# Kernel tuning notes

Measured on AMD Instinct MI355X. Metric: run time of the kernel, lower is better.

The kernel has to match this reference:

```python
import jax, jax.numpy as jnp
import numpy as np

N = 50000        # nodes per type (MiRNA=0, Disease=1, LncRNA=2)
E = 500000       # edges per relation
F_IN, HID, OUT = 128, 64, 64
ITEMS, SIZE, T = 4096, 4096, 100
# relation order: MvsD, DvsM, MvsL, LvsM, LvsD, DvsL
SRC = (0, 1, 0, 2, 2, 1)
DST = (1, 0, 2, 0, 1, 2)


def _sage_hetero_layer(h, edges, Wp, bp, Ws, bs, Wn):
    """One HeteroGraphConv(SAGEConv pool, aggregate='sum') layer.
    h: list of 3 [N, Fin] node-feature arrays; edges: [6, 2, E] int."""
    n = h[0].shape[0]
    out = [None, None, None]
    for e in range(6):
        s, d = SRC[e], DST[e]
        pooled = jax.nn.relu(h[s] @ Wp[e] + bp[e])                 # [N, Fin]
        msg = pooled[edges[e, 0]]                                  # [E, Fin] gather at src
        agg = jax.ops.segment_max(msg, edges[e, 1], num_segments=n)
        agg = jnp.where(jnp.isneginf(agg), 0.0, agg)               # DGL: 0 for isolated dst
        o = h[d] @ Ws[e] + bs[e] + agg @ Wn[e]                     # fc_self(+bias) + fc_neigh
        out[d] = o if out[d] is None else out[d] + o
    return out


def setup_inputs() -> dict:
    key = jax.random.key(0)
    ks = jax.random.split(key, 32)
    s = 0.05
    inp = {
        'hM': jax.random.normal(ks[0], (N, F_IN), jnp.float32),
        'hD': jax.random.normal(ks[1], (N, F_IN), jnp.float32),
        'hL': jax.random.normal(ks[2], (N, F_IN), jnp.float32),
        'Wpool1': jax.random.normal(ks[3], (6, F_IN, F_IN), jnp.float32) * s,
        'bpool1': jnp.zeros((6, F_IN), jnp.float32),
        'Wself1': jax.random.normal(ks[4], (6, F_IN, HID), jnp.float32) * s,
        'bself1': jnp.zeros((6, HID), jnp.float32),
        'Wneigh1': jax.random.normal(ks[5], (6, F_IN, HID), jnp.float32) * s,
        'Wpool2': jax.random.normal(ks[6], (6, HID, HID), jnp.float32) * s,
        'bpool2': jnp.zeros((6, HID), jnp.float32),
        'Wself2': jax.random.normal(ks[7], (6, HID, HID), jnp.float32) * s,
        'bself2': jnp.zeros((6, HID), jnp.float32),
        'Wneigh2': jax.random.normal(ks[8], (6, HID, HID), jnp.float32) * s,
        'Wpool3': jax.random.normal(ks[9], (6, HID, HID), jnp.float32) * s,
        'bpool3': jnp.zeros((6, HID), jnp.float32),
        'Wself3': jax.random.normal(ks[10], (6, HID, OUT), jnp.float32) * s,
        'bself3': jnp.zeros((6, OUT), jnp.float32),
        'Wneigh3': jax.random.normal(ks[11], (6, HID, OUT), jnp.float32) * s,
        'Adj': jax.random.uniform(ks[12], (SIZE, ITEMS), jnp.float32),
        'noise': jax.random.normal(ks[13], (N, OUT), jnp.float32),
        'W1': jax.random.normal(ks[14], (ITEMS + OUT, 256), jnp.float32) * s,
        'b1': jnp.zeros((256,), jnp.float32),
        'W2': jax.random.normal(ks[15], (256, 512), jnp.float32) * s,
        'b2': jnp.zeros((512,), jnp.float32),
        'W3': jax.random.normal(ks[16], (512, 1024), jnp.float32) * s,
        'b3': jnp.zeros((1024,), jnp.float32),
        'W4': jax.random.normal(ks[17], (1024, ITEMS), jnp.float32) * s,
        'b4': jnp.zeros((ITEMS,), jnp.float32),
        'edges': jax.random.randint(ks[18], (6, 2, E), 0, N, jnp.int32),
        't': 50,
        'size': SIZE,
        'leftIndex': 0,
    }
    return inp


def reference(hM, hD, hL, Wpool1, bpool1, Wself1, bself1, Wneigh1,
              Wpool2, bpool2, Wself2, bself2, Wneigh2,
              Wpool3, bpool3, Wself3, bself3, Wneigh3,
              Adj, noise, W1, b1, W2, b2, W3, b3, W4, b4,
              edges, t, size, leftIndex):
    h1 = _sage_hetero_layer([hM, hD, hL], edges, Wpool1, bpool1, Wself1, bself1, Wneigh1)
    h2 = _sage_hetero_layer(h1, edges, Wpool2, bpool2, Wself2, bself2, Wneigh2)
    h3 = _sage_hetero_layer(h2, edges, Wpool3, bpool3, Wself3, bself3, Wneigh3)
    mirna = h3[0]                                                  # [N, OUT]
    mirna = mirna / jnp.maximum(jnp.sum(jnp.abs(mirna), axis=1, keepdims=True), 1e-12)
    # diffusion schedule
    betas = jnp.linspace(1e-4, 0.02, T, dtype=jnp.float32)
    alpha_bars = jnp.cumprod(1.0 - betas)
    signal_rates = jnp.sqrt(alpha_bars)
    noise_rates = jnp.sqrt(1.0 - alpha_bars)
    noisy = signal_rates[t] * mirna + noise_rates[t] * noise
    fake = jax.lax.stop_gradient(noisy[leftIndex:leftIndex + size])  # detach + slice
    M = jnp.concatenate([Adj, fake], axis=1)                       # [size, ITEMS+OUT]
    x = jax.nn.relu(M @ W1 + b1)
    x = jax.nn.relu(x @ W2 + b2)
    x = jax.nn.relu(x @ W3 + b3)
    x = jax.nn.sigmoid(x @ W4 + b4)
    return fake, x
```

## Files before the change

kernel.cpp:

```cpp
#include <hip/hip_runtime.h>
#include <hip/hip_bf16.h>

#define NNODE 50000
#define NEDGE 500000
#define SZ    4096
#define NBKT  256
#define BWID  196
#define BCAP  4096
#define RELEB ((size_t)NBKT * BCAP)
#define ZK1   8

typedef __attribute__((ext_vector_type(8))) short bf16x8;
typedef __attribute__((ext_vector_type(4))) float f32x4;

__device__ __forceinline__ float bits2f(unsigned short u) {
    return __uint_as_float(((unsigned)u) << 16);
}
__device__ __forceinline__ unsigned short f2bits(float f) {
    unsigned x = __float_as_uint(f);
    unsigned r = x + 0x7fffu + ((x >> 16) & 1u);
    return (unsigned short)(r >> 16);
}
__device__ __forceinline__ unsigned pk_max_u16(unsigned a, unsigned b) {
    unsigned lo = max(a & 0xffffu, b & 0xffffu);
    unsigned hi = max(a >> 16, b >> 16);
    return lo | (hi << 16);
}
__device__ __forceinline__ void gl_lds16(const void* g, void* l) {
    __builtin_amdgcn_global_load_lds(
        (const __attribute__((address_space(1))) unsigned int*)g,
        (__attribute__((address_space(3))) unsigned int*)l, 16, 0, 0);
}

template<int RELU, int SIG, int OUTF32, int PART, int PIPE>
__global__ __launch_bounds__(256)
void gemm128(const unsigned short* __restrict__ A, const unsigned short* __restrict__ Bt,
             const float* __restrict__ bias, void* __restrict__ Cv, int M, int N, int K)
{
    __shared__ unsigned short As[PIPE + 1][128 * 64];
    __shared__ unsigned short Bs[PIPE + 1][128 * 64];
    const int tid = threadIdx.x;
    const int wave = tid >> 6, lane = tid & 63;
    const int m16 = lane & 15, quad = lane >> 4;
    const int wr = wave >> 1, wc = wave & 1;
    const int nwg = gridDim.x * gridDim.y;
    int bid = blockIdx.y * gridDim.x + blockIdx.x;
    if ((nwg & 7) == 0) { int cpx = nwg >> 3; bid = (bid & 7) * cpx + (bid >> 3); }
    const int bx = bid % gridDim.x, by = bid / gridDim.x;
    const int row0 = by * 128, col0 = bx * 128;
    const int lrow = lane >> 3, lcol = (lane & 7) * 8;

    f32x4 acc[4][4] = {};

    int k0beg = 0, k0end = K;
    if (PART) {
        const int per = ((K >> 6) + gridDim.z - 1) / gridDim.z;
        k0beg = blockIdx.z * per * 64;
        k0end = min(K, k0beg + per * 64);
    }
    const int nt = (k0end - k0beg) >> 6;

    auto STAGE = [&](int b, int k0) {
#pragma unroll
        for (int i = 0; i < 4; ++i) {
            int chunk = wave * 4 + i;
            int row = chunk * 8 + lrow;
            gl_lds16(A  + (size_t)(row0 + row) * K + k0 + lcol, &As[b][chunk * 512]);
            gl_lds16(Bt + (size_t)(col0 + row) * K + k0 + lcol, &Bs[b][chunk * 512]);
        }
    };
    auto COMPUTE = [&](int b) {
#pragma unroll
        for (int ks = 0; ks < 2; ++ks) {
            bf16x8 a[4], bb[4];
#pragma unroll
            for (int mt = 0; mt < 4; ++mt)
                a[mt] = *(const bf16x8*)&As[b][(wr * 64 + mt * 16 + m16) * 64 + ks * 32 + quad * 8];
#pragma unroll
            for (int nt2 = 0; nt2 < 4; ++nt2)
                bb[nt2] = *(const bf16x8*)&Bs[b][(wc * 64 + nt2 * 16 + m16) * 64 + ks * 32 + quad * 8];
#pragma unroll
            for (int mt = 0; mt < 4; ++mt)
#pragma unroll
                for (int nt2 = 0; nt2 < 4; ++nt2)
                    acc[mt][nt2] = __builtin_amdgcn_mfma_f32_16x16x32_bf16(a[mt], bb[nt2], acc[mt][nt2], 0, 0, 0);
        }
    };

    if (PIPE) {
        STAGE(0, k0beg);
        __syncthreads();
        int cur = 0;
        for (int t = 0; t < nt; ++t) {
            if (t + 1 < nt) STAGE(cur ^ 1, k0beg + (t + 1) * 64);
            COMPUTE(cur);
            __syncthreads();
            cur ^= 1;
        }
    } else {
        for (int t = 0; t < nt; ++t) {
            STAGE(0, k0beg + t * 64);
            __syncthreads();
            COMPUTE(0);
            __syncthreads();
        }
    }

    if (PART) {
        float* P = (float*)Cv + (size_t)blockIdx.z * M * N;
#pragma unroll
        for (int mt = 0; mt < 4; ++mt)
#pragma unroll
            for (int nt2 = 0; nt2 < 4; ++nt2) {
                int gc = col0 + wc * 64 + nt2 * 16 + m16;
#pragma unroll
                for (int r = 0; r < 4; ++r) {
                    int gm = row0 + wr * 64 + mt * 16 + quad * 4 + r;
                    P[(size_t)gm * N + gc] = acc[mt][nt2][r];
                }
            }
        return;
    }

#pragma unroll
    for (int mt = 0; mt < 4; ++mt) {
#pragma unroll
        for (int nt2 = 0; nt2 < 4; ++nt2) {
            int gc = col0 + wc * 64 + nt2 * 16 + m16;
            float bv = bias[gc];
#pragma unroll
            for (int r = 0; r < 4; ++r) {
                int gm = row0 + wr * 64 + mt * 16 + quad * 4 + r;
                size_t idx = (size_t)gm * N + gc;
                float v = acc[mt][nt2][r] + bv;
                if (RELU) v = fmaxf(v, 0.f);
                if (SIG)  v = 1.f / (1.f + __expf(-v));
                if (OUTF32) ((float*)Cv)[idx] = v;
                else        ((unsigned short*)Cv)[idx] = f2bits(v);
            }
        }
    }
}

__global__ __launch_bounds__(256)
void mlp1_ep_k(const float* __restrict__ p, const float* __restrict__ b1,
               unsigned short* __restrict__ x1)
{
    const size_t MN = (size_t)SZ * 256;
    int i = blockIdx.x * 256 + threadIdx.x;
    if (i >= (int)(MN / 4)) return;
    float4 s = ((const float4*)p)[i];
#pragma unroll
    for (int z = 1; z < ZK1; ++z) {
        float4 a = ((const float4*)(p + (size_t)z * MN))[i];
        s.x += a.x; s.y += a.y; s.z += a.z; s.w += a.w;
    }
    int base = i * 4;
    ushort4 o;
    o.x = f2bits(fmaxf(s.x + b1[(base + 0) & 255], 0.f));
    o.y = f2bits(fmaxf(s.y + b1[(base + 1) & 255], 0.f));
    o.z = f2bits(fmaxf(s.z + b1[(base + 2) & 255], 0.f));
    o.w = f2bits(fmaxf(s.w + b1[(base + 3) & 255], 0.f));
    ((ushort4*)x1)[i] = o;
}

template<int NT>
__global__ __launch_bounds__(256)
void pool2_k(const unsigned short* __restrict__ A0, const unsigned short* __restrict__ A1,
             const unsigned short* __restrict__ Bt0, const unsigned short* __restrict__ Bt1,
             const float* __restrict__ b0, const float* __restrict__ b1,
             unsigned short* __restrict__ out, int M, int K)
{
    __shared__ unsigned short As[64][72];
    __shared__ unsigned short Bs[NT * 16][72];
    const int z = blockIdx.z;
    const unsigned short* A = z ? A1 : A0;
    const unsigned short* Bt = z ? Bt1 : Bt0;
    const float* bias = z ? b1 : b0;
    const int N = NT * 16;
    unsigned short* Cv = out + (size_t)z * M * N;

    const int tid = threadIdx.x;
    const int wave = tid >> 6, lane = tid & 63;
    const int m16 = lane & 15, quad = lane >> 4;
    const int row0 = blockIdx.y * 64, col0 = blockIdx.x * N;

    f32x4 acc[NT] = {};

    for (int k0 = 0; k0 < K; k0 += 64) {
#pragma unroll
        for (int it = 0; it < 2; ++it) {
            int u = tid + it * 256;
            int m = u >> 3, c = (u & 7) * 8;
            int gm = row0 + m;
            uint4 v = make_uint4(0u, 0u, 0u, 0u);
            if (gm < M) v = *(const uint4*)(A + (size_t)gm * K + k0 + c);
            *(uint4*)&As[m][c] = v;
        }
#pragma unroll
        for (int it = 0; it < NT / 2; ++it) {
            int u = tid + it * 256;
            int n = u >> 3, c = (u & 7) * 8;
            uint4 v = *(const uint4*)(Bt + (size_t)(col0 + n) * K + k0 + c);
            *(uint4*)&Bs[n][c] = v;
        }
        __syncthreads();
#pragma unroll
        for (int ks = 0; ks < 2; ++ks) {
            bf16x8 a = *(const bf16x8*)&As[wave * 16 + m16][ks * 32 + quad * 8];
#pragma unroll
            for (int nt = 0; nt < NT; ++nt) {
                bf16x8 b = *(const bf16x8*)&Bs[nt * 16 + m16][ks * 32 + quad * 8];
                acc[nt] = __builtin_amdgcn_mfma_f32_16x16x32_bf16(a, b, acc[nt], 0, 0, 0);
            }
        }
        __syncthreads();
    }

#pragma unroll
    for (int nt = 0; nt < NT; ++nt) {
        int gc = col0 + nt * 16 + m16;
        float bv = bias[gc];
#pragma unroll
        for (int r = 0; r < 4; ++r) {
            int gm = row0 + wave * 16 + quad * 4 + r;
            if (gm < M)
                Cv[(size_t)gm * N + gc] = f2bits(fmaxf(acc[nt][r] + bv, 0.f));
        }
    }
}

__global__ __launch_bounds__(256)
void pool6_k(const unsigned short* __restrict__ hin, const unsigned short* __restrict__ pT,
             const float* __restrict__ bp, unsigned short* __restrict__ pooled6, int M)
{
    const int SRCr[6] = {0, 1, 0, 2, 2, 1};
    __shared__ unsigned short As[64][72];
    __shared__ unsigned short Bs[64][72];
    const int z = blockIdx.z;
    const unsigned short* A = hin + (size_t)SRCr[z] * M * 64;
    const unsigned short* Bt = pT + (size_t)z * 4096;
    const float* bias = bp + z * 64;
    unsigned short* Cv = pooled6 + (size_t)z * M * 64;

    const int tid = threadIdx.x;
    const int wave = tid >> 6, lane = tid & 63;
    const int m16 = lane & 15, quad = lane >> 4;
    const int row0 = blockIdx.y * 64;

    f32x4 acc[4] = {};

    {
#pragma unroll
        for (int it = 0; it < 2; ++it) {
            int u = tid + it * 256;
            int m = u >> 3, c = (u & 7) * 8;
            int gm = row0 + m;
            uint4 v = make_uint4(0u, 0u, 0u, 0u);
            if (gm < M) v = *(const uint4*)(A + (size_t)gm * 64 + c);
            *(uint4*)&As[m][c] = v;
        }
#pragma unroll
        for (int it = 0; it < 2; ++it) {
            int u = tid + it * 256;
            int n = u >> 3, c = (u & 7) * 8;
            uint4 v = *(const uint4*)(Bt + (size_t)n * 64 + c);
            *(uint4*)&Bs[n][c] = v;
        }
        __syncthreads();
#pragma unroll
        for (int ks = 0; ks < 2; ++ks) {
            bf16x8 a = *(const bf16x8*)&As[wave * 16 + m16][ks * 32 + quad * 8];
#pragma unroll
            for (int nt = 0; nt < 4; ++nt) {
                bf16x8 b = *(const bf16x8*)&Bs[nt * 16 + m16][ks * 32 + quad * 8];
                acc[nt] = __builtin_amdgcn_mfma_f32_16x16x32_bf16(a, b, acc[nt], 0, 0, 0);
            }
        }
    }

#pragma unroll
    for (int nt = 0; nt < 4; ++nt) {
        int gc = nt * 16 + m16;
        float bv = bias[gc];
#pragma unroll
        for (int r = 0; r < 4; ++r) {
            int gm = row0 + wave * 16 + quad * 4 + r;
            if (gm < M)
                Cv[(size_t)gm * 64 + gc] = f2bits(fmaxf(acc[nt][r] + bv, 0.f));
        }
    }
}

template<int NT>
__global__ __launch_bounds__(256)
void mfma_gemm(const unsigned short* __restrict__ A1, const unsigned short* __restrict__ A2,
               const unsigned short* __restrict__ A3,
               const unsigned short* __restrict__ Bt, const float* __restrict__ bias,
               const float* __restrict__ bias2,
               unsigned short* __restrict__ Cv, int M, int N, int Ka, int Kb, int Kc)
{
    __shared__ unsigned short As[64][72];
    __shared__ unsigned short Bs[NT * 16][72];
    const int tid = threadIdx.x;
    const int wave = tid >> 6, lane = tid & 63;
    const int m16 = lane & 15, quad = lane >> 4;
    const int row0 = blockIdx.y * 64, col0 = blockIdx.x * (NT * 16);
    const int K = Ka + Kb + Kc;

    f32x4 acc[NT] = {};

    for (int k0 = 0; k0 < K; k0 += 64) {
        const int seg = (k0 >= Ka + Kb) ? 2 : ((k0 >= Ka) ? 1 : 0);
        const unsigned short* src = seg == 2 ? A3 : (seg == 1 ? A2 : A1);
        const int ld = seg == 2 ? Kc : (seg == 1 ? Kb : Ka);
        const int kb = k0 - (seg == 2 ? Ka + Kb : (seg == 1 ? Ka : 0));
#pragma unroll
        for (int it = 0; it < 2; ++it) {
            int u = tid + it * 256;
            int m = u >> 3, c = (u & 7) * 8;
            int gm = row0 + m;
            uint4 v = make_uint4(0u, 0u, 0u, 0u);
            if (gm < M) v = *(const uint4*)(src + (size_t)gm * ld + kb + c);
            *(uint4*)&As[m][c] = v;
        }
#pragma unroll
        for (int it = 0; it < NT / 2; ++it) {
            int u = tid + it * 256;
            int n = u >> 3, c = (u & 7) * 8;
            uint4 v = *(const uint4*)(Bt + (size_t)(col0 + n) * K + k0 + c);
            *(uint4*)&Bs[n][c] = v;
        }
        __syncthreads();
#pragma unroll
        for (int ks = 0; ks < 2; ++ks) {
            bf16x8 a = *(const bf16x8*)&As[wave * 16 + m16][ks * 32 + quad * 8];
#pragma unroll
            for (int nt = 0; nt < NT; ++nt) {
                bf16x8 b = *(const bf16x8*)&Bs[nt * 16 + m16][ks * 32 + quad * 8];
                acc[nt] = __builtin_amdgcn_mfma_f32_16x16x32_bf16(a, b, acc[nt], 0, 0, 0);
            }
        }
        __syncthreads();
    }

#pragma unroll
    for (int nt = 0; nt < NT; ++nt) {
        int gc = col0 + nt * 16 + m16;
        float bv = bias[gc] + bias2[gc];
#pragma unroll
        for (int r = 0; r < 4; ++r) {
            int gm = row0 + wave * 16 + quad * 4 + r;
            if (gm < M)
                Cv[(size_t)gm * N + gc] = f2bits(acc[nt][r] + bv);
        }
    }
}

__global__ __launch_bounds__(256)
void fused3_k(const unsigned short* __restrict__ hin,
              const unsigned short* __restrict__ regA, const unsigned short* __restrict__ regB,
              const unsigned short* __restrict__ fT, const float* __restrict__ bs,
              unsigned short* __restrict__ hout, int M)
{
    const int PAe[3] = {1, 0, 2}, PBe[3] = {3, 4, 5};
    __shared__ unsigned short As[64][72];
    __shared__ unsigned short Bs[64][72];
    const int z = blockIdx.z;
    const int eA = PAe[z], eB = PBe[z];
    const unsigned short* A1 = hin + (size_t)z * M * 64;
    const unsigned short* A2 = (eA < 4) ? regA + (size_t)eA * M * 64 : regB + (size_t)(eA - 4) * M * 64;
    const unsigned short* A3 = (eB < 4) ? regA + (size_t)eB * M * 64 : regB + (size_t)(eB - 4) * M * 64;
    const unsigned short* Bt = fT + (size_t)z * 12288;
    const float* bias = bs + eA * 64;
    const float* bias2 = bs + eB * 64;
    unsigned short* Cv = hout + (size_t)z * M * 64;

    const int tid = threadIdx.x;
    const int wave = tid >> 6, lane = tid & 63;
    const int m16 = lane & 15, quad = lane >> 4;
    const int row0 = blockIdx.y * 64;

    f32x4 acc[4] = {};

#pragma unroll
    for (int seg = 0; seg < 3; ++seg) {
        const unsigned short* src = seg == 2 ? A3 : (seg == 1 ? A2 : A1);
        const int k0 = seg * 64;
#pragma unroll
        for (int it = 0; it < 2; ++it) {
            int u = tid + it * 256;
            int m = u >> 3, c = (u & 7) * 8;
            int gm = row0 + m;
            uint4 v = make_uint4(0u, 0u, 0u, 0u);
            if (gm < M) v = *(const uint4*)(src + (size_t)gm * 64 + c);
            *(uint4*)&As[m][c] = v;
        }
#pragma unroll
        for (int it = 0; it < 2; ++it) {
            int u = tid + it * 256;
            int n = u >> 3, c = (u & 7) * 8;
            uint4 v = *(const uint4*)(Bt + (size_t)n * 192 + k0 + c);
            *(uint4*)&Bs[n][c] = v;
        }
        __syncthreads();
#pragma unroll
        for (int ks = 0; ks < 2; ++ks) {
            bf16x8 a = *(const bf16x8*)&As[wave * 16 + m16][ks * 32 + quad * 8];
#pragma unroll
            for (int nt = 0; nt < 4; ++nt) {
                bf16x8 b = *(const bf16x8*)&Bs[nt * 16 + m16][ks * 32 + quad * 8];
                acc[nt] = __builtin_amdgcn_mfma_f32_16x16x32_bf16(a, b, acc[nt], 0, 0, 0);
            }
        }
        __syncthreads();
    }

#pragma unroll
    for (int nt = 0; nt < 4; ++nt) {
        int gc = nt * 16 + m16;
        float bv = bias[gc] + bias2[gc];
#pragma unroll
        for (int r = 0; r < 4; ++r) {
            int gm = row0 + wave * 16 + quad * 4 + r;
            if (gm < M)
                Cv[(size_t)gm * 64 + gc] = f2bits(acc[nt][r] + bv);
        }
    }
}

__global__ __launch_bounds__(256)
void transpose_cvt(const float* __restrict__ src1, const float* __restrict__ src2,
                   unsigned short* __restrict__ dst, int R1, int R2, int Nn)
{
    __shared__ float tile[32][33];
    const int R = R1 + R2;
    const int e = blockIdx.z;
    src1 += (size_t)e * R1 * Nn;
    if (src2) src2 += (size_t)e * R2 * Nn;
    dst += (size_t)e * Nn * R;
    const int r0 = blockIdx.x * 32, n0 = blockIdx.y * 32;
    const int lr = threadIdx.x >> 5, ln = threadIdx.x & 31;
#pragma unroll
    for (int i = 0; i < 4; ++i) {
        int r = r0 + lr + i * 8, n = n0 + ln;
        float v = 0.f;
        if (r < R && n < Nn) v = (r < R1) ? src1[(size_t)r * Nn + n]
                                          : src2[(size_t)(r - R1) * Nn + n];
        tile[lr + i * 8][ln] = v;
    }
    __syncthreads();
#pragma unroll
    for (int i = 0; i < 4; ++i) {
        int n = n0 + lr + i * 8, r = r0 + ln;
        if (n < Nn && r < R) dst[(size_t)n * R + r] = f2bits(tile[ln][lr + i * 8]);
    }
}

__global__ __launch_bounds__(256)
void fuse_w_k(const float* __restrict__ Ws, const float* __restrict__ Wn,
              unsigned short* __restrict__ dst, int F)
{
    const int PAe[3] = {1, 0, 2}, PBe[3] = {3, 4, 5};
    __shared__ float tile[32][33];
    const int p = blockIdx.z;
    const int eA = PAe[p], eB = PBe[p];
    const int Kt = 3 * F;
    unsigned short* D = dst + (size_t)p * 64 * Kt;
    const int r0 = blockIdx.x * 32;
    const int n0 = blockIdx.y * 32;
    const int lr = threadIdx.x >> 5, ln = threadIdx.x & 31;
    for (int seg = 0; seg < 3; ++seg) {
        __syncthreads();
#pragma unroll
        for (int i = 0; i < 4; ++i) {
            int r = r0 + lr + i * 8, n = n0 + ln;
            float v;
            if (seg == 0)
                v = Ws[((size_t)eA * F + r) * 64 + n] + Ws[((size_t)eB * F + r) * 64 + n];
            else if (seg == 1)
                v = Wn[((size_t)eA * F + r) * 64 + n];
            else
                v = Wn[((size_t)eB * F + r) * 64 + n];
            tile[lr + i * 8][ln] = v;
        }
        __syncthreads();
        const int koff = seg * F;
#pragma unroll
        for (int i = 0; i < 4; ++i) {
            int n = n0 + lr + i * 8, r = r0 + ln;
            D[(size_t)n * Kt + koff + r] = f2bits(tile[ln][lr + i * 8]);
        }
    }
}

__global__ __launch_bounds__(256)
void cvt3_k(const float* __restrict__ s0, const float* __restrict__ s1,
            const float* __restrict__ s2, unsigned short* __restrict__ dst)
{
    const int z = blockIdx.z;
    const float* src = z == 0 ? s0 : (z == 1 ? s1 : s2);
    dst += (size_t)z * NNODE * 128;
    int i = blockIdx.x * 256 + threadIdx.x;
    if (i >= 1600000) return;
    float4 v = ((const float4*)src)[i];
    ushort4 w;
    w.x = f2bits(v.x); w.y = f2bits(v.y); w.z = f2bits(v.z); w.w = f2bits(v.w);
    ((ushort4*)dst)[i] = w;
}

__global__ __launch_bounds__(256)
void cvt_adj_k(const float* __restrict__ src, unsigned short* __restrict__ dst)
{
    int i = blockIdx.x * 256 + threadIdx.x;
    if (i >= 4194304) return;
    int r = i >> 10, c4 = i & 1023;
    float4 v = ((const float4*)src)[i];
    ushort4 w;
    w.x = f2bits(v.x); w.y = f2bits(v.y); w.z = f2bits(v.z); w.w = f2bits(v.w);
    *(ushort4*)(dst + (size_t)r * 4160 + c4 * 4) = w;
}

__global__ __launch_bounds__(256)
void binit_k(int* __restrict__ bcur)
{
    bcur[blockIdx.x * NBKT + threadIdx.x] = threadIdx.x * BCAP;
}

__global__ __launch_bounds__(256)
void bucket_k(const int* __restrict__ edges, int* __restrict__ bcur,
              unsigned* __restrict__ ebuf)
{
    const int r = blockIdx.y;
    const int base = blockIdx.x * 4096;
    const int tid = threadIdx.x;
    __shared__ int lcnt[NBKT];
    __shared__ int lbase[NBKT];
    for (int i = tid; i < NBKT; i += 256) lcnt[i] = 0;
    __syncthreads();
    unsigned ent[16];
    int rnk[16];
#pragma unroll
    for (int i = 0; i < 16; ++i) {
        int e = base + tid + i * 256;
        ent[i] = 0xffffffffu;
        rnk[i] = 0;
        if (e < NEDGE) {
            int src = edges[(size_t)r * 2 * NEDGE + e];
            int dst = edges[(size_t)r * 2 * NEDGE + NEDGE + e];
            ent[i] = ((unsigned)dst << 16) | (unsigned)src;
            rnk[i] = atomicAdd(&lcnt[dst / BWID], 1);
        }
    }
    __syncthreads();
    for (int i = tid; i < NBKT; i += 256)
        lbase[i] = lcnt[i] ? atomicAdd(&bcur[r * NBKT + i], lcnt[i]) : 0;
    __syncthreads();
#pragma unroll
    for (int i = 0; i < 16; ++i)
        if (ent[i] != 0xffffffffu) {
            int b = (int)(ent[i] >> 16) / BWID;
            int pos = lbase[b] + rnk[i];
            if (pos < (b + 1) * BCAP)
                ebuf[(size_t)r * RELEB + pos] = ent[i];
        }
}

__global__ __launch_bounds__(256)
void bscan_k(const int* __restrict__ bcur, int* __restrict__ bbase,
             int* __restrict__ offs)
{
    const int r = blockIdx.x, tid = threadIdx.x;
    const int lane = tid & 63, wv = tid >> 6;
    int v = bcur[r * NBKT + tid] - tid * BCAP;
    if (v > BCAP) v = BCAP;
    int x = v;
#pragma unroll
    for (int off = 1; off < 64; off <<= 1) {
        int t = __shfl_up(x, off);
        if (lane >= off) x += t;
    }
    __shared__ int wsum[4];
    if (lane == 63) wsum[wv] = x;
    __syncthreads();
    int add = 0;
#pragma unroll
    for (int w = 0; w < 4; ++w) if (w < wv) add += wsum[w];
    x += add;
    bbase[r * NBKT + tid] = x - v;
    if (tid == 255) offs[(size_t)r * (NNODE + 1) + NNODE] = x;
}

__global__ __launch_bounds__(256)
void debucket_k(const unsigned* __restrict__ ebuf, const int* __restrict__ bcur,
                const int* __restrict__ bbase, int* __restrict__ offs,
                unsigned short* __restrict__ srcs)
{
    const int r = blockIdx.y, b = blockIdx.x, tid = threadIdx.x;
    const int lo = b * BWID;
    __shared__ unsigned es[BCAP];
    __shared__ unsigned short stage[BCAP];
    __shared__ int lhist[256];
    __shared__ int buf[256];
    __shared__ int lcur[256];
    int cnt = bcur[r * NBKT + b] - b * BCAP;
    if (cnt > BCAP) cnt = BCAP;
    const int base = bbase[r * NBKT + b];
    lhist[tid] = 0;
    __syncthreads();
    for (int j = tid; j < cnt; j += 256) {
        unsigned e = ebuf[(size_t)r * RELEB + (size_t)b * BCAP + j];
        es[j] = e;
        atomicAdd(&lhist[(int)(e >> 16) - lo], 1);
    }
    __syncthreads();
    int v = lhist[tid];
    buf[tid] = v;
    __syncthreads();
    for (int off = 1; off < 256; off <<= 1) {
        int t = (tid >= off) ? buf[tid - off] : 0;
        __syncthreads();
        buf[tid] += t;
        __syncthreads();
    }
    int excl = buf[tid] - v;
    int node = lo + tid;
    if (tid < BWID && node < NNODE) offs[(size_t)r * (NNODE + 1) + node] = base + excl;
    lcur[tid] = excl;
    __syncthreads();
    for (int j = tid; j < cnt; j += 256) {
        unsigned e = es[j];
        int d = (int)(e >> 16) - lo;
        int p = atomicAdd(&lcur[d], 1);
        stage[p] = (unsigned short)(e & 0xffffu);
    }
    __syncthreads();
    for (int j = tid; j < cnt; j += 256)
        srcs[(size_t)r * NEDGE + base + j] = stage[j];
}

template<int F>
__global__ __launch_bounds__(256)
void gather2_k(const unsigned short* __restrict__ pooled, const int* __restrict__ offs,
               const unsigned short* __restrict__ srcs, unsigned short* __restrict__ agg,
               int e0, int e1)
{
    const int CG = F / 8;
    const int z = blockIdx.z;
    const int e = z ? e1 : e0;
    pooled += (size_t)z * NNODE * F;
    agg    += (size_t)z * NNODE * F;
    offs   += (size_t)e * (NNODE + 1);
    srcs   += (size_t)e * NEDGE;
    int idx = blockIdx.x * 256 + threadIdx.x;
    int n = idx / CG, cg = idx % CG;
    if (n >= NNODE) return;
    int beg = offs[n], end = offs[n + 1];
    unsigned m0 = 0, m1 = 0, m2 = 0, m3 = 0;
    int j = beg;
    for (; j + 4 <= end; j += 4) {
        int s0 = srcs[j], s1 = srcs[j + 1], s2 = srcs[j + 2], s3 = srcs[j + 3];
        uint4 v0 = *(const uint4*)(pooled + (size_t)s0 * F + cg * 8);
        uint4 v1 = *(const uint4*)(pooled + (size_t)s1 * F + cg * 8);
        uint4 v2 = *(const uint4*)(pooled + (size_t)s2 * F + cg * 8);
        uint4 v3 = *(const uint4*)(pooled + (size_t)s3 * F + cg * 8);
        m0 = pk_max_u16(m0, pk_max_u16(pk_max_u16(v0.x, v1.x), pk_max_u16(v2.x, v3.x)));
        m1 = pk_max_u16(m1, pk_max_u16(pk_max_u16(v0.y, v1.y), pk_max_u16(v2.y, v3.y)));
        m2 = pk_max_u16(m2, pk_max_u16(pk_max_u16(v0.z, v1.z), pk_max_u16(v2.z, v3.z)));
        m3 = pk_max_u16(m3, pk_max_u16(pk_max_u16(v0.w, v1.w), pk_max_u16(v2.w, v3.w)));
    }
    for (; j < end; ++j) {
        int s = srcs[j];
        uint4 v = *(const uint4*)(pooled + (size_t)s * F + cg * 8);
        m0 = pk_max_u16(m0, v.x);
        m1 = pk_max_u16(m1, v.y);
        m2 = pk_max_u16(m2, v.z);
        m3 = pk_max_u16(m3, v.w);
    }
    uint4 o; o.x = m0; o.y = m1; o.z = m2; o.w = m3;
    *(uint4*)(agg + (size_t)n * F + cg * 8) = o;
}

__global__ __launch_bounds__(256)
void gather6_k(const unsigned short* __restrict__ pooled6, const int* __restrict__ offs,
               const unsigned short* __restrict__ srcs,
               unsigned short* __restrict__ regA, unsigned short* __restrict__ regB)
{
    const int F = 64, CG = 8;
    const int z = blockIdx.z;
    const unsigned short* pooled = pooled6 + (size_t)z * NNODE * F;
    unsigned short* agg = (z < 4) ? regA + (size_t)z * NNODE * F
                                  : regB + (size_t)(z - 4) * NNODE * F;
    offs += (size_t)z * (NNODE + 1);
    srcs += (size_t)z * NEDGE;
    int idx = blockIdx.x * 256 + threadIdx.x;
    int n = idx / CG, cg = idx % CG;
    if (n >= NNODE) return;
    int beg = offs[n], end = offs[n + 1];
    unsigned m0 = 0, m1 = 0, m2 = 0, m3 = 0;
    int j = beg;
    for (; j + 4 <= end; j += 4) {
        int s0 = srcs[j], s1 = srcs[j + 1], s2 = srcs[j + 2], s3 = srcs[j + 3];
        uint4 v0 = *(const uint4*)(pooled + (size_t)s0 * F + cg * 8);
        uint4 v1 = *(const uint4*)(pooled + (size_t)s1 * F + cg * 8);
        uint4 v2 = *(const uint4*)(pooled + (size_t)s2 * F + cg * 8);
        uint4 v3 = *(const uint4*)(pooled + (size_t)s3 * F + cg * 8);
        m0 = pk_max_u16(m0, pk_max_u16(pk_max_u16(v0.x, v1.x), pk_max_u16(v2.x, v3.x)));
        m1 = pk_max_u16(m1, pk_max_u16(pk_max_u16(v0.y, v1.y), pk_max_u16(v2.y, v3.y)));
        m2 = pk_max_u16(m2, pk_max_u16(pk_max_u16(v0.z, v1.z), pk_max_u16(v2.z, v3.z)));
        m3 = pk_max_u16(m3, pk_max_u16(pk_max_u16(v0.w, v1.w), pk_max_u16(v2.w, v3.w)));
    }
    for (; j < end; ++j) {
        int s = srcs[j];
        uint4 v = *(const uint4*)(pooled + (size_t)s * F + cg * 8);
        m0 = pk_max_u16(m0, v.x);
        m1 = pk_max_u16(m1, v.y);
        m2 = pk_max_u16(m2, v.z);
        m3 = pk_max_u16(m3, v.w);
    }
    uint4 o; o.x = m0; o.y = m1; o.z = m2; o.w = m3;
    *(uint4*)(agg + (size_t)n * F + cg * 8) = o;
}

__global__ __launch_bounds__(64)
void fake_k(const unsigned short* __restrict__ mirna, const float* __restrict__ noise,
            const int* __restrict__ t_p, const int* __restrict__ left_p,
            unsigned short* __restrict__ adj_s, float* __restrict__ fake_out)
{
    int r = blockIdx.x, c = threadIdx.x;
    int t = *t_p, left = *left_p;
    int row = left + r;
    float x = bits2f(mirna[(size_t)row * 64 + c]);
    float s = fabsf(x);
#pragma unroll
    for (int off = 32; off > 0; off >>= 1) s += __shfl_down(s, off);
    s = __shfl(s, 0);
    float ab = 1.f;
    for (int i = 0; i <= t; ++i)
        ab *= (1.f - (1e-4f + (0.02f - 1e-4f) * ((float)i / 99.f)));
    float v = sqrtf(ab) * (x / fmaxf(s, 1e-12f)) + sqrtf(1.f - ab) * noise[(size_t)row * 64 + c];
    adj_s[(size_t)r * 4160 + 4096 + c] = f2bits(v);
    fake_out[(size_t)r * 64 + c] = v;
}

extern "C" void kernel_launch(void* const* d_in, const int* in_sizes, int n_in,
                              void* d_out, int out_size, void* d_ws, size_t ws_size,
                              hipStream_t stream)
{
    const float* h0[3]    = {(const float*)d_in[0], (const float*)d_in[1], (const float*)d_in[2]};
    const float* Wpool[3] = {(const float*)d_in[3], (const float*)d_in[8],  (const float*)d_in[13]};
    const float* bpool[3] = {(const float*)d_in[4], (const float*)d_in[9],  (const float*)d_in[14]};
    const float* bself[3] = {(const float*)d_in[6], (const float*)d_in[11], (const float*)d_in[16]};
    const float* Wself[3] = {(const float*)d_in[5], (const float*)d_in[10], (const float*)d_in[15]};
    const float* Wneigh[3]= {(const float*)d_in[7], (const float*)d_in[12], (const float*)d_in[17]};
    const float* Adj   = (const float*)d_in[18];
    const float* noise = (const float*)d_in[19];
    const float* W1 = (const float*)d_in[20]; const float* b1 = (const float*)d_in[21];
    const float* W2 = (const float*)d_in[22]; const float* b2 = (const float*)d_in[23];
    const float* W3 = (const float*)d_in[24]; const float* b3 = (const float*)d_in[25];
    const float* W4 = (const float*)d_in[26]; const float* b4 = (const float*)d_in[27];
    const int* edges  = (const int*)d_in[28];
    const int* t_p    = (const int*)d_in[29];
    const int* left_p = (const int*)d_in[31];

    unsigned short* ws = (unsigned short*)d_ws;
    const size_t P1 = 0, P2 = 98304, P3 = 122880;
    const size_t FU1 = 147456, FU2 = 245760, FU3 = 294912;
    const size_t W1T = 344064, W2T = 1409024, W3T = 1540096, W4T = 2064384;
    const size_t ADJ = 6258688;
    const size_t POOLED = 23298048;
    const size_t HA = 36098048, HB = 45698048;
    int* bcur  = (int*)(ws + 55298048);
    int* bbase = bcur + 6 * NBKT;
    int* offs  = bbase + 6 * NBKT;
    unsigned short* srcs = (unsigned short*)(offs + 6 * (NNODE + 1));
    unsigned* ebuf = (unsigned*)(ws + POOLED);
    unsigned short* x1 = ws + POOLED;
    unsigned short* x2 = x1 + (size_t)SZ * 256;
    unsigned short* x3 = x2 + (size_t)SZ * 512;
    unsigned short* adj_s = ws + ADJ;
    float* out_fake = (float*)d_out;
    float* out_x    = out_fake + (size_t)SZ * 64;
    unsigned short* hb0 = (unsigned short*)out_x;
    unsigned short* agg2_l1 = hb0 + 19200000;
    unsigned short* pooled6 = (unsigned short*)out_x;
    unsigned short* aggB6 = pooled6 + 19200000;
    unsigned short* aggA6 = ws + POOLED;
    float* x1p = out_x;

    const int SRCr[6] = {0, 1, 0, 2, 2, 1};
    const int PAe[3] = {1, 0, 2}, PBe[3] = {3, 4, 5};
    dim3 T(256);

    transpose_cvt<<<dim3(4, 4, 6),   T, 0, stream>>>(Wpool[0], nullptr, ws + P1, 128, 0, 128);
    transpose_cvt<<<dim3(2, 2, 6),   T, 0, stream>>>(Wpool[1], nullptr, ws + P2, 64, 0, 64);
    transpose_cvt<<<dim3(2, 2, 6),   T, 0, stream>>>(Wpool[2], nullptr, ws + P3, 64, 0, 64);
    fuse_w_k<<<dim3(4, 2, 3), T, 0, stream>>>(Wself[0], Wneigh[0], ws + FU1, 128);
    fuse_w_k<<<dim3(2, 2, 3), T, 0, stream>>>(Wself[1], Wneigh[1], ws + FU2, 64);
    fuse_w_k<<<dim3(2, 2, 3), T, 0, stream>>>(Wself[2], Wneigh[2], ws + FU3, 64);
    transpose_cvt<<<dim3(130, 8, 1), T, 0, stream>>>(W1, nullptr, ws + W1T, 4160, 0, 256);
    transpose_cvt<<<dim3(8, 16, 1),  T, 0, stream>>>(W2, nullptr, ws + W2T, 256, 0, 512);
    transpose_cvt<<<dim3(16, 32, 1), T, 0, stream>>>(W3, nullptr, ws + W3T, 512, 0, 1024);
    transpose_cvt<<<dim3(32, 128, 1),T, 0, stream>>>(W4, nullptr, ws + W4T, 1024, 0, 4096);
    cvt_adj_k<<<16384, T, 0, stream>>>(Adj, adj_s);
    cvt3_k<<<dim3(6250, 1, 3), T, 0, stream>>>(h0[0], h0[1], h0[2], hb0);

    binit_k<<<6, T, 0, stream>>>(bcur);
    bucket_k<<<dim3(123, 6), T, 0, stream>>>(edges, bcur, ebuf);
    bscan_k<<<6, T, 0, stream>>>(bcur, bbase, offs);
    debucket_k<<<dim3(NBKT, 6), T, 0, stream>>>(ebuf, bcur, bbase, offs, srcs);

    for (int p = 0; p < 3; ++p) {
        const int eA = PAe[p], eB = PBe[p];
        pool2_k<8><<<dim3(1, 782, 2), T, 0, stream>>>(
            hb0 + (size_t)SRCr[eA] * NNODE * 128, hb0 + (size_t)SRCr[eB] * NNODE * 128,
            ws + P1 + (size_t)eA * 16384, ws + P1 + (size_t)eB * 16384,
            bpool[0] + eA * 128, bpool[0] + eB * 128,
            ws + POOLED, NNODE, 128);
        gather2_k<128><<<dim3(3125, 1, 2), T, 0, stream>>>(
            ws + POOLED, offs, srcs, agg2_l1, eA, eB);
        mfma_gemm<4><<<dim3(1, 782), T, 0, stream>>>(
            hb0 + (size_t)p * NNODE * 128, agg2_l1, agg2_l1 + (size_t)NNODE * 128,
            ws + FU1 + (size_t)p * 24576, bself[0] + eA * 64, bself[0] + eB * 64,
            ws + HA + (size_t)p * NNODE * 64, NNODE, 64, 128, 128, 128);
    }

    unsigned short* hin = ws + HA;
    unsigned short* hout = ws + HB;
    for (int layer = 1; layer <= 2; ++layer) {
        const unsigned short* pT = ws + (layer == 1 ? P2 : P3);
        const unsigned short* fT = ws + (layer == 1 ? FU2 : FU3);
        pool6_k<<<dim3(1, 782, 6), T, 0, stream>>>(hin, pT, bpool[layer], pooled6, NNODE);
        gather6_k<<<dim3(1563, 1, 6), T, 0, stream>>>(pooled6, offs, srcs, aggA6, aggB6);
        fused3_k<<<dim3(1, 782, 3), T, 0, stream>>>(hin, aggA6, aggB6, fT,
                                                    bself[layer], hout, NNODE);
        unsigned short* tmp = hin; hin = hout; hout = tmp;
    }

    fake_k<<<SZ, dim3(64), 0, stream>>>(hin, noise, t_p, left_p, adj_s, out_fake);

    gemm128<0, 0, 0, 1, 1><<<dim3(2, 32, ZK1), T, 0, stream>>>(
        adj_s, ws + W1T, b1, x1p, SZ, 256, 4160);
    mlp1_ep_k<<<1024, T, 0, stream>>>(x1p, b1, x1);
    gemm128<1, 0, 0, 0, 1><<<dim3(4, 32),  T, 0, stream>>>(x1, ws + W2T, b2, x2, SZ, 512, 256);
    gemm128<1, 0, 0, 0, 1><<<dim3(8, 32),  T, 0, stream>>>(x2, ws + W3T, b3, x3, SZ, 1024, 512);
    gemm128<0, 1, 1, 0, 0><<<dim3(32, 32), T, 0, stream>>>(x3, ws + W4T, b4, out_x, SZ, 4096, 1024);
}
```

Baseline: 884.8 us.

## Batch weight-conversion launches, deepen gather unroll, shrink bucket capacity, split final GEMM

Merges several small weight transpose/fuse launches into combined grids, including a new kernel that converts W2, W3 and W4 together. This cuts the number of kernel launches. The gather2 loop is unrolled from 4 to 8 edges to expose more memory-level parallelism. BCAP drops from 4096 to 2560, which shrinks the bucket workspace but risks overflow if a bucket gets more edges. The last GEMM is split into two half-width launches, which adds a launch and gives no clear benefit.

After: 868.7 us. About the same (-1.8%).

```diff
diff --git a/kernel.cpp b/kernel.cpp
--- a/kernel.cpp
+++ b/kernel.cpp
@@ -6,7 +6,7 @@
 #define SZ    4096
 #define NBKT  256
 #define BWID  196
-#define BCAP  4096
+#define BCAP  2560
 #define RELEB ((size_t)NBKT * BCAP)
 #define ZK1   8
 
@@ -431,22 +431,55 @@
 
 __global__ __launch_bounds__(256)
 void transpose_cvt(const float* __restrict__ src1, const float* __restrict__ src2,
-                   unsigned short* __restrict__ dst, int R1, int R2, int Nn)
+                   unsigned short* __restrict__ dst, int R1, int R2, int Nn,
+                   const float* __restrict__ src1b, unsigned short* __restrict__ dstb)
 {
     __shared__ float tile[32][33];
     const int R = R1 + R2;
-    const int e = blockIdx.z;
-    src1 += (size_t)e * R1 * Nn;
-    if (src2) src2 += (size_t)e * R2 * Nn;
-    dst += (size_t)e * Nn * R;
+    int e = blockIdx.z;
+    const float* s1 = src1;
+    unsigned short* d = dst;
+    if (src1b && e >= 6) { s1 = src1b; d = dstb; e -= 6; }
+    s1 += (size_t)e * R1 * Nn;
+    const float* s2 = src2 ? src2 + (size_t)e * R2 * Nn : nullptr;
+    d += (size_t)e * Nn * R;
     const int r0 = blockIdx.x * 32, n0 = blockIdx.y * 32;
     const int lr = threadIdx.x >> 5, ln = threadIdx.x & 31;
 #pragma unroll
     for (int i = 0; i < 4; ++i) {
         int r = r0 + lr + i * 8, n = n0 + ln;
         float v = 0.f;
-        if (r < R && n < Nn) v = (r < R1) ? src1[(size_t)r * Nn + n]
-                                          : src2[(size_t)(r - R1) * Nn + n];
+        if (r < R && n < Nn) v = (r < R1) ? s1[(size_t)r * Nn + n]
+                                          : s2[(size_t)(r - R1) * Nn + n];
+        tile[lr + i * 8][ln] = v;
+    }
+    __syncthreads();
+#pragma unroll
+    for (int i = 0; i < 4; ++i) {
+        int n = n0 + lr + i * 8, r = r0 + ln;
+        if (n < Nn && r < R) d[(size_t)n * R + r] = f2bits(tile[ln][lr + i * 8]);
+    }
+}
+
+__global__ __launch_bounds__(256)
+void tcvt_mlp_k(const float* __restrict__ W2, const float* __restrict__ W3,
+                const float* __restrict__ W4, unsigned short* __restrict__ d2,
+                unsigned short* __restrict__ d3, unsigned short* __restrict__ d4)
+{
+    const int z = blockIdx.z;
+    const float* src; unsigned short* dst; int R, Nn, gx, gy;
+    if (z == 0)      { src = W2; dst = d2; R = 256;  Nn = 512;  gx = 8;  gy = 16; }
+    else if (z == 1) { src = W3; dst = d3; R = 512;  Nn = 1024; gx = 16; gy = 32; }
+    else             { src = W4; dst = d4; R = 1024; Nn = 4096; gx = 32; gy = 128; }
+    if (blockIdx.x >= (unsigned)gx || blockIdx.y >= (unsigned)gy) return;
+    __shared__ float tile[32][33];
+    const int r0 = blockIdx.x * 32, n0 = blockIdx.y * 32;
+    const int lr = threadIdx.x >> 5, ln = threadIdx.x & 31;
+#pragma unroll
+    for (int i = 0; i < 4; ++i) {
+        int r = r0 + lr + i * 8, n = n0 + ln;
+        float v = 0.f;
+        if (r < R && n < Nn) v = src[(size_t)r * Nn + n];
         tile[lr + i * 8][ln] = v;
     }
     __syncthreads();
@@ -459,14 +492,18 @@
 
 __global__ __launch_bounds__(256)
 void fuse_w_k(const float* __restrict__ Ws, const float* __restrict__ Wn,
-              unsigned short* __restrict__ dst, int F)
+              unsigned short* __restrict__ dst, int F,
+              const float* __restrict__ Wsb, const float* __restrict__ Wnb,
+              unsigned short* __restrict__ dstb)
 {
     const int PAe[3] = {1, 0, 2}, PBe[3] = {3, 4, 5};
     __shared__ float tile[32][33];
-    const int p = blockIdx.z;
+    int p = blockIdx.z;
+    const float* ws_ = Ws; const float* wn_ = Wn; unsigned short* db = dst;
+    if (Wsb && p >= 3) { ws_ = Wsb; wn_ = Wnb; db = dstb; p -= 3; }
     const int eA = PAe[p], eB = PBe[p];
     const int Kt = 3 * F;
-    unsigned short* D = dst + (size_t)p * 64 * Kt;
+    unsigned short* D = db + (size_t)p * 64 * Kt;
     const int r0 = blockIdx.x * 32;
     const int n0 = blockIdx.y * 32;
     const int lr = threadIdx.x >> 5, ln = threadIdx.x & 31;
@@ -477,11 +514,11 @@
             int r = r0 + lr + i * 8, n = n0 + ln;
             float v;
             if (seg == 0)
-                v = Ws[((size_t)eA * F + r) * 64 + n] + Ws[((size_t)eB * F + r) * 64 + n];
+                v = ws_[((size_t)eA * F + r) * 64 + n] + ws_[((size_t)eB * F + r) * 64 + n];
             else if (seg == 1)
-                v = Wn[((size_t)eA * F + r) * 64 + n];
+                v = wn_[((size_t)eA * F + r) * 64 + n];
             else
-                v = Wn[((size_t)eB * F + r) * 64 + n];
+                v = wn_[((size_t)eB * F + r) * 64 + n];
             tile[lr + i * 8][ln] = v;
         }
         __syncthreads();
@@ -658,16 +695,23 @@
     int beg = offs[n], end = offs[n + 1];
     unsigned m0 = 0, m1 = 0, m2 = 0, m3 = 0;
     int j = beg;
-    for (; j + 4 <= end; j += 4) {
-        int s0 = srcs[j], s1 = srcs[j + 1], s2 = srcs[j + 2], s3 = srcs[j + 3];
-        uint4 v0 = *(const uint4*)(pooled + (size_t)s0 * F + cg * 8);
-        uint4 v1 = *(const uint4*)(pooled + (size_t)s1 * F + cg * 8);
-        uint4 v2 = *(const uint4*)(pooled + (size_t)s2 * F + cg * 8);
-        uint4 v3 = *(const uint4*)(pooled + (size_t)s3 * F + cg * 8);
-        m0 = pk_max_u16(m0, pk_max_u16(pk_max_u16(v0.x, v1.x), pk_max_u16(v2.x, v3.x)));
-        m1 = pk_max_u16(m1, pk_max_u16(pk_max_u16(v0.y, v1.y), pk_max_u16(v2.y, v3.y)));
-        m2 = pk_max_u16(m2, pk_max_u16(pk_max_u16(v0.z, v1.z), pk_max_u16(v2.z, v3.z)));
-        m3 = pk_max_u16(m3, pk_max_u16(pk_max_u16(v0.w, v1.w), pk_max_u16(v2.w, v3.w)));
+    for (; j + 8 <= end; j += 8) {
+        uint4 v0 = *(const uint4*)(pooled + (size_t)srcs[j + 0] * F + cg * 8);
+        uint4 v1 = *(const uint4*)(pooled + (size_t)srcs[j + 1] * F + cg * 8);
+        uint4 v2 = *(const uint4*)(pooled + (size_t)srcs[j + 2] * F + cg * 8);
+        uint4 v3 = *(const uint4*)(pooled + (size_t)srcs[j + 3] * F + cg * 8);
+        uint4 v4 = *(const uint4*)(pooled + (size_t)srcs[j + 4] * F + cg * 8);
+        uint4 v5 = *(const uint4*)(pooled + (size_t)srcs[j + 5] * F + cg * 8);
+        uint4 v6 = *(const uint4*)(pooled + (size_t)srcs[j + 6] * F + cg * 8);
+        uint4 v7 = *(const uint4*)(pooled + (size_t)srcs[j + 7] * F + cg * 8);
+        m0 = pk_max_u16(m0, pk_max_u16(pk_max_u16(pk_max_u16(v0.x, v1.x), pk_max_u16(v2.x, v3.x)),
+                                       pk_max_u16(pk_max_u16(v4.x, v5.x), pk_max_u16(v6.x, v7.x))));
+        m1 = pk_max_u16(m1, pk_max_u16(pk_max_u16(pk_max_u16(v0.y, v1.y), pk_max_u16(v2.y, v3.y)),
+                                       pk_max_u16(pk_max_u16(v4.y, v5.y), pk_max_u16(v6.y, v7.y))));
+        m2 = pk_max_u16(m2, pk_max_u16(pk_max_u16(pk_max_u16(v0.z, v1.z), pk_max_u16(v2.z, v3.z)),
+                                       pk_max_u16(pk_max_u16(v4.z, v5.z), pk_max_u16(v6.z, v7.z))));
+        m3 = pk_max_u16(m3, pk_max_u16(pk_max_u16(pk_max_u16(v0.w, v1.w), pk_max_u16(v2.w, v3.w)),
+                                       pk_max_u16(pk_max_u16(v4.w, v5.w), pk_max_u16(v6.w, v7.w))));
     }
     for (; j < end; ++j) {
         int s = srcs[j];
@@ -792,16 +836,17 @@
     const int PAe[3] = {1, 0, 2}, PBe[3] = {3, 4, 5};
     dim3 T(256);
 
-    transpose_cvt<<<dim3(4, 4, 6),   T, 0, stream>>>(Wpool[0], nullptr, ws + P1, 128, 0, 128);
-    transpose_cvt<<<dim3(2, 2, 6),   T, 0, stream>>>(Wpool[1], nullptr, ws + P2, 64, 0, 64);
-    transpose_cvt<<<dim3(2, 2, 6),   T, 0, stream>>>(Wpool[2], nullptr, ws + P3, 64, 0, 64);
-    fuse_w_k<<<dim3(4, 2, 3), T, 0, stream>>>(Wself[0], Wneigh[0], ws + FU1, 128);
-    fuse_w_k<<<dim3(2, 2, 3), T, 0, stream>>>(Wself[1], Wneigh[1], ws + FU2, 64);
-    fuse_w_k<<<dim3(2, 2, 3), T, 0, stream>>>(Wself[2], Wneigh[2], ws + FU3, 64);
-    transpose_cvt<<<dim3(130, 8, 1), T, 0, stream>>>(W1, nullptr, ws + W1T, 4160, 0, 256);
-    transpose_cvt<<<dim3(8, 16, 1),  T, 0, stream>>>(W2, nullptr, ws + W2T, 256, 0, 512);
-    transpose_cvt<<<dim3(16, 32, 1), T, 0, stream>>>(W3, nullptr, ws + W3T, 512, 0, 1024);
-    transpose_cvt<<<dim3(32, 128, 1),T, 0, stream>>>(W4, nullptr, ws + W4T, 1024, 0, 4096);
+    transpose_cvt<<<dim3(4, 4, 6), T, 0, stream>>>(Wpool[0], nullptr, ws + P1, 128, 0, 128,
+                                                   nullptr, nullptr);
+    transpose_cvt<<<dim3(2, 2, 12), T, 0, stream>>>(Wpool[1], nullptr, ws + P2, 64, 0, 64,
+                                                    Wpool[2], ws + P3);
+    fuse_w_k<<<dim3(4, 2, 3), T, 0, stream>>>(Wself[0], Wneigh[0], ws + FU1, 128,
+                                              nullptr, nullptr, nullptr);
+    fuse_w_k<<<dim3(2, 2, 6), T, 0, stream>>>(Wself[1], Wneigh[1], ws + FU2, 64,
+                                              Wself[2], Wneigh[2], ws + FU3);
+    transpose_cvt<<<dim3(130, 8, 1), T, 0, stream>>>(W1, nullptr, ws + W1T, 4160, 0, 256,
+                                                     nullptr, nullptr);
+    tcvt_mlp_k<<<dim3(32, 128, 3), T, 0, stream>>>(W2, W3, W4, ws + W2T, ws + W3T, ws + W4T);
     cvt_adj_k<<<16384, T, 0, stream>>>(Adj, adj_s);
     cvt3_k<<<dim3(6250, 1, 3), T, 0, stream>>>(h0[0], h0[1], h0[2], hb0);
 
@@ -844,5 +889,8 @@
     mlp1_ep_k<<<1024, T, 0, stream>>>(x1p, b1, x1);
     gemm128<1, 0, 0, 0, 1><<<dim3(4, 32),  T, 0, stream>>>(x1, ws + W2T, b2, x2, SZ, 512, 256);
     gemm128<1, 0, 0, 0, 1><<<dim3(8, 32),  T, 0, stream>>>(x2, ws + W3T, b3, x3, SZ, 1024, 512);
-    gemm128<0, 1, 1, 0, 0><<<dim3(32, 32), T, 0, stream>>>(x3, ws + W4T, b4, out_x, SZ, 4096, 1024);
-}
+    gemm128<0, 1, 1, 0, 0><<<dim3(16, 32), T, 0, stream>>>(
+        x3, ws + W4T, b4, out_x, SZ, 4096, 1024);
+    gemm128<0, 1, 1, 0, 0><<<dim3(16, 32), T, 0, stream>>>(
+        x3, ws + W4T + (size_t)2048 * 1024, b4 + 2048, out_x + 2048, SZ, 4096, 1024);
+}
```
